# Kernel optimization log

Hardware: AMD Instinct MI355X
Metric: run time of the kernel (lower is better)

## Reference

```python
import jax, jax.numpy as jnp
import numpy as np

NUM_HEADS = 8
SCALE = 25.0
SIM_THRESH = 0.75


def setup_inputs() -> dict:
    key = jax.random.key(0)
    ks = jax.random.split(key, 6)
    B, N, C = 1, 2048, 1024
    x_cls = jax.random.normal(ks[0], (B, N, C), jnp.float32)
    x_reg = jax.random.normal(ks[1], (B, N, C), jnp.float32)
    cls_score = jax.random.uniform(ks[2], (N,), jnp.float32)
    fg_score = jax.random.uniform(ks[3], (N,), jnp.float32)
    W_qkv_cls = jax.random.normal(ks[4], (3 * C, C), jnp.float32) * 0.02
    W_qkv_reg = jax.random.normal(ks[5], (3 * C, C), jnp.float32) * 0.02
    return {"x_cls": x_cls, "x_reg": x_reg, "cls_score": cls_score,
            "fg_score": fg_score, "W_qkv_cls": W_qkv_cls, "W_qkv_reg": W_qkv_reg}


def _l2norm(t):
    return t / jnp.linalg.norm(t, axis=-1, keepdims=True)


def reference(x_cls, x_reg, cls_score, fg_score, W_qkv_cls, W_qkv_reg):
    B, N, C = x_cls.shape
    H = NUM_HEADS
    d = C // H

    def qkv(x, W):
        # (B,N,3C) -> (3,B,H,N,d)
        t = (x @ W.T).reshape(B, N, 3, H, d).transpose(2, 0, 3, 1, 4)
        return t[0], t[1], t[2]

    q_cls, k_cls, v_cls = qkv(x_cls, W_qkv_cls)
    q_reg, k_reg, _ = qkv(x_reg, W_qkv_reg)

    q_cls, k_cls = _l2norm(q_cls), _l2norm(k_cls)
    q_reg, k_reg = _l2norm(q_reg), _l2norm(k_reg)
    v_cls_normed = _l2norm(v_cls)

    # scores broadcast: s[..., i, j] = score[j]; transpose -> score[i]
    s_cls = cls_score.reshape(1, 1, 1, N)
    s_fg = fg_score.reshape(1, 1, 1, N)
    # use_mask=True branch
    m_cls = (s_cls > jnp.swapaxes(s_cls, -2, -1) - 0.1).astype(x_cls.dtype)
    m_fg = (s_fg > jnp.swapaxes(s_fg, -2, -1) - 0.1).astype(x_cls.dtype)

    attn_cls_raw = jnp.einsum('bhid,bhjd->bhij', v_cls_normed, v_cls_normed)

    attn_cls = jax.nn.softmax(
        jnp.einsum('bhid,bhjd->bhij', q_cls, k_cls) * SCALE * s_cls * m_cls, axis=-1)
    attn_reg = jax.nn.softmax(
        jnp.einsum('bhid,bhjd->bhij', q_reg, k_reg) * SCALE * s_fg * m_fg, axis=-1)
    attn = (attn_reg + attn_cls) * 0.5

    x = jnp.einsum('bhij,bhjd->bhid', attn, v_cls).transpose(0, 2, 1, 3).reshape(B, N, C)
    x_ori = v_cls.transpose(0, 2, 1, 3).reshape(B, N, C)
    x_out = jnp.concatenate([x, x_ori], axis=-1)  # (B, N, 2C)

    # ave=True branch (batch 0, head-mean)
    raw = attn_cls_raw.sum(axis=1)[0] / H  # (N, N)
    sim_mask = (raw > SIM_THRESH).astype(x_cls.dtype)
    sim_attn = attn.sum(axis=1)[0] / H
    sim_round2 = jax.nn.softmax(sim_attn, axis=-1)
    sim_round2 = sim_mask * sim_round2
    sim_round2 = sim_round2 / jnp.sum(sim_round2, axis=-1, keepdims=True)
    return x_out, sim_round2
```

## Files before the change

kernel.cpp:

```cpp
#include <hip/hip_runtime.h>


#define NTOK 2048
#define CDIM 1024
#define OD   5120

typedef __attribute__((ext_vector_type(8))) short bf16x8;
typedef __attribute__((ext_vector_type(4))) short s16x4;
typedef __attribute__((ext_vector_type(2))) short s16x2;
typedef __attribute__((ext_vector_type(4))) float f32x4;

#define MFMA16(a,b,c) __builtin_amdgcn_mfma_f32_16x16x32_bf16((a),(b),(c),0,0,0)

__device__ __forceinline__ short f2bf(float x){
  unsigned u = __float_as_uint(x);
  u += 0x7FFFu + ((u >> 16) & 1u);
  return (short)(u >> 16);
}

__device__ __forceinline__ void atomAddF(float* p, float v){
  unsafeAtomicAdd(p, v);
}

__device__ __forceinline__ void gld16(const short* g, short* l){
  __builtin_amdgcn_global_load_lds(
      (const __attribute__((address_space(1))) unsigned int*)g,
      (__attribute__((address_space(3))) unsigned int*)l, 16, 0, 0);
}

__global__ __launch_bounds__(256,2) void k_qkv(
    const float* __restrict__ xcls, const float* __restrict__ xreg,
    const float* __restrict__ Wcls, const float* __restrict__ Wreg,
    float* __restrict__ tmp)
{
  const int m0 = blockIdx.x * 64;
  const int o0 = blockIdx.y * 64;
  const float* X; const float* W; int wrow;
  if (o0 < 3072){ X = xcls; W = Wcls; wrow = o0; }
  else          { X = xreg; W = Wreg; wrow = o0 - 3072; }

  __shared__ short As[64][40];
  __shared__ short Bs[64][40];

  const int tid  = threadIdx.x;
  const int lane = tid & 63;
  const int wid  = tid >> 6;
  const int wm   = (wid >> 1) * 32;
  const int wo   = (wid & 1) * 32;
  const int fr   = lane & 15;
  const int fk   = (lane >> 4) * 8;

  f32x4 acc[2][2] = {};

  for (int k0 = 0; k0 < CDIM; k0 += 32){
    #pragma unroll
    for (int it = 0; it < 2; ++it){
      int idx = tid + it*256;
      int r = idx >> 3;
      int c = (idx & 7) << 2;
      float4 xv = *(const float4*)(X + (size_t)(m0+r)*CDIM + k0 + c);
      *(s16x4*)&As[r][c] = (s16x4){ f2bf(xv.x), f2bf(xv.y), f2bf(xv.z), f2bf(xv.w) };
      float4 wv = *(const float4*)(W + (size_t)(wrow+r)*CDIM + k0 + c);
      *(s16x4*)&Bs[r][c] = (s16x4){ f2bf(wv.x), f2bf(wv.y), f2bf(wv.z), f2bf(wv.w) };
    }
    __syncthreads();
    bf16x8 a0 = *(const bf16x8*)&As[wm      + fr][fk];
    bf16x8 a1 = *(const bf16x8*)&As[wm + 16 + fr][fk];
    bf16x8 b0 = *(const bf16x8*)&Bs[wo      + fr][fk];
    bf16x8 b1 = *(const bf16x8*)&Bs[wo + 16 + fr][fk];
    acc[0][0] = MFMA16(a0,b0,acc[0][0]);
    acc[0][1] = MFMA16(a0,b1,acc[0][1]);
    acc[1][0] = MFMA16(a1,b0,acc[1][0]);
    acc[1][1] = MFMA16(a1,b1,acc[1][1]);
    __syncthreads();
  }
  #pragma unroll
  for (int fi=0;fi<2;fi++)
    #pragma unroll
    for (int fj=0;fj<2;fj++)
      #pragma unroll
      for (int r=0;r<4;r++){
        int mm = m0 + wm + fi*16 + (lane>>4)*4 + r;
        int oo = o0 + wo + fj*16 + fr;
        tmp[(size_t)mm*OD + oo] = acc[fi][fj][r];
      }
}

__global__ __launch_bounds__(256,4) void k_norm(
    const float* __restrict__ tmp, float* __restrict__ out,
    short* __restrict__ qc, short* __restrict__ kc,
    short* __restrict__ qr, short* __restrict__ kr,
    short* __restrict__ vn, short* __restrict__ vb)
{
  int task = blockIdx.x*4 + (threadIdx.x>>6);
  int lane = threadIdx.x & 63;
  int n = task / 40;
  int rem = task - n*40;
  int chunk = rem >> 3;
  int h = rem & 7;
  const float* src = tmp + (size_t)n*OD + (chunk<<10) + h*128;
  float2 v = *(const float2*)(src + lane*2);
  float ss = v.x*v.x + v.y*v.y;
  #pragma unroll
  for (int m=1;m<64;m<<=1) ss += __shfl_xor(ss, m);
  float rn = 1.0f / sqrtf(ss);
  size_t base = ((size_t)h*NTOK + n)*128 + lane*2;
  s16x2 nv = { f2bf(v.x*rn), f2bf(v.y*rn) };
  switch(chunk){
    case 0: *(s16x2*)&qc[base] = nv; break;
    case 1: *(s16x2*)&kc[base] = nv; break;
    case 3: *(s16x2*)&qr[base] = nv; break;
    case 4: *(s16x2*)&kr[base] = nv; break;
    default: {
      *(s16x2*)&vn[base] = nv;
      *(s16x2*)&vb[base] = (s16x2){ f2bf(v.x), f2bf(v.y) };
      *(float2*)&out[(size_t)n*2048 + 1024 + h*128 + lane*2] = v;
      break;
    }
  }
}

__global__ __launch_bounds__(256,4) void k_vT(
    const short* __restrict__ vb, short* __restrict__ vT)
{
  int b = blockIdx.x;
  int h  = b >> 6;
  int nt = (b >> 1) & 31;
  int dt = b & 1;
  __shared__ short t[64][72];
  int tid = threadIdx.x;
  int r  = tid >> 2;
  int c0 = (tid & 3) << 4;
  #pragma unroll
  for (int u=0;u<2;u++){
    bf16x8 val = *(const bf16x8*)&vb[((size_t)h*NTOK + nt*64 + r)*128 + dt*64 + c0 + u*8];
    #pragma unroll
    for (int e=0;e<8;e++) t[r][c0+u*8+e] = val[e];
  }
  __syncthreads();
  #pragma unroll
  for (int u=0;u<2;u++){
    bf16x8 o;
    #pragma unroll
    for (int e=0;e<8;e++) o[e] = t[c0+u*8+e][r];
    *(bf16x8*)&vT[((size_t)h*128 + dt*64 + r)*NTOK + nt*64 + c0 + u*8] = o;
  }
}

#define JLEN 1024

__global__ __launch_bounds__(256,2) void k_attn(
    const short* __restrict__ qc, const short* __restrict__ kc,
    const short* __restrict__ qr, const short* __restrict__ kr,
    const short* __restrict__ vT,
    const float* __restrict__ csc, const float* __restrict__ fsc,
    float* __restrict__ s_cls, float* __restrict__ s_reg,
    float* __restrict__ Up)
{
  const int tid = threadIdx.x;
  const int l   = tid & 63;
  const int w   = tid >> 6;
  const int L    = blockIdx.x;
  const int xcd  = L & 7;
  const int slot = L >> 3;
  const int hs   = ((slot >> 5) << 3) | xcd;
  const int h    = hs >> 1;
  const int s    = hs & 1;
  const int rem  = slot & 31;
  const int js   = rem >> 4;
  const int ib   = rem & 15;

  const int iw  = ib * 128 + w * 32;
  const int fr  = l & 15;
  const int fk8 = (l >> 4) * 8;
  const size_t hN = (size_t)h * NTOK;
  const size_t hD = (size_t)h * 128;

  const short* Qp = s ? qr : qc;
  const short* Kp = s ? kr : kc;
  const float* sc = s ? fsc : csc;
  float* ssum     = s ? s_reg : s_cls;
  float* Ub       = Up + (size_t)(js*2 + s) * 2097152;

  __shared__ __align__(16) short Kbuf[2][4][4][64][8];
  __shared__ __align__(16) short Vbuf[2][8][2][64][8];
  __shared__ __align__(16) short Ebuf[4][2][2][64][8];

  const int t8 = w * 8;

#define STAGE(DB, JN) do {                                                   \
    _Pragma("unroll")                                                        \
    for (int q8=0; q8<8; ++q8){                                              \
      int t = t8 + q8;                                                       \
      if (t < 16){                                                           \
        int jf = t >> 2, kk = t & 3;                                         \
        gld16(Kp + (hN + (JN) + jf*16 + fr)*128 + kk*32 + fk8,               \
              &Kbuf[DB][jf][kk][0][0]);                                      \
      } else {                                                               \
        int u = t - 16, df = u >> 1, ks = u & 1;                             \
        gld16(vT + (hD + df*16 + fr)*2048 + (JN) + ks*32 + fk8,              \
              &Vbuf[DB][df][ks][0][0]);                                      \
      }                                                                      \
    }                                                                        \
  } while(0)

  bf16x8 aq[2][4];
  #pragma unroll
  for (int i2=0;i2<2;i2++)
    #pragma unroll
    for (int kk=0;kk<4;kk++)
      aq[i2][kk] = *(const bf16x8*)&Qp[(hN + iw + i2*16 + fr)*128 + kk*32 + fk8];

  float sci[2][4];
  #pragma unroll
  for (int i2=0;i2<2;i2++)
    #pragma unroll
    for (int r=0;r<4;r++)
      sci[i2][r] = sc[iw + i2*16 + (l>>4)*4 + r];

  f32x4 U[2][8] = {};
  float p[2][4] = {};

  const int ebyte = l & 7;
  const int ehi   = (l >> 3) & 1;
  const int jbase = js * JLEN;

  STAGE(0, jbase);
  __syncthreads();

  for (int jt = 0; jt < 16; ++jt){
    const int db = jt & 1;
    const int j0 = jbase + jt*64;
    if (jt < 15){ if (db) STAGE(0, j0 + 64); else STAGE(1, j0 + 64); }
    #pragma unroll
    for (int jf=0; jf<4; ++jf){
      f32x4 S0 = {}; f32x4 S1 = {};
      #pragma unroll
      for (int kk=0; kk<4; ++kk){
        bf16x8 b = *(const bf16x8*)&Kbuf[db][jf][kk][l][0];
        S0 = MFMA16(aq[0][kk], b, S0);
        S1 = MFMA16(aq[1][kk], b, S1);
      }
      float sj = sc[j0 + jf*16 + fr];
      float sj25 = 25.0f * sj;
      const int ks  = jf >> 1;
      const int sub = ((jf & 1) << 1) | ehi;
      #pragma unroll
      for (int r=0;r<4;r++){
        float e0 = (sj > sci[0][r]-0.1f) ? __expf(S0[r]*sj25) : 1.0f;
        float e1 = (sj > sci[1][r]-0.1f) ? __expf(S1[r]*sj25) : 1.0f;
        p[0][r] += e0; p[1][r] += e1;
        int lrow = (l>>4)*4 + r + (sub<<4);
        Ebuf[w][0][ks][lrow][ebyte] = f2bf(e0);
        Ebuf[w][1][ks][lrow][ebyte] = f2bf(e1);
      }
    }
    #pragma unroll
    for (int ks=0; ks<2; ++ks){
      bf16x8 ef0 = *(const bf16x8*)&Ebuf[w][0][ks][l][0];
      bf16x8 ef1 = *(const bf16x8*)&Ebuf[w][1][ks][l][0];
      #pragma unroll
      for (int df=0; df<8; ++df){
        bf16x8 bv = *(const bf16x8*)&Vbuf[db][df][ks][l][0];
        U[0][df] = MFMA16(ef0, bv, U[0][df]);
        U[1][df] = MFMA16(ef1, bv, U[1][df]);
      }
    }
    __syncthreads();
  }
#undef STAGE

  #pragma unroll
  for (int m=1;m<16;m<<=1)
    #pragma unroll
    for (int i2=0;i2<2;i2++)
      #pragma unroll
      for (int r=0;r<4;r++) p[i2][r] += __shfl_xor(p[i2][r], m);
  if (fr == 0){
    #pragma unroll
    for (int i2=0;i2<2;i2++)
      #pragma unroll
      for (int r=0;r<4;r++)
        atomAddF(&ssum[hN + iw + i2*16 + (l>>4)*4 + r], p[i2][r]);
  }
  #pragma unroll
  for (int i2=0;i2<2;i2++)
    #pragma unroll
    for (int df=0;df<8;df++)
      #pragma unroll
      for (int r=0;r<4;r++)
        Ub[(hN + iw + i2*16 + (l>>4)*4 + r)*128 + df*16 + fr] = U[i2][df][r];
}

__global__ __launch_bounds__(256,8) void k_attn_fin(
    const float* __restrict__ Up,
    const float* __restrict__ s_cls, const float* __restrict__ s_reg,
    float* __restrict__ out)
{
  int task = blockIdx.x*4 + (threadIdx.x>>6);
  int lane = threadIdx.x & 63;
  int h = task >> 11;
  int row = task & 2047;
  size_t b = (size_t)task*128 + lane*2;
  float2 c0 = *(const float2*)(Up + 0*2097152 + b);
  float2 r0 = *(const float2*)(Up + 1*2097152 + b);
  float2 c1 = *(const float2*)(Up + 2*2097152 + b);
  float2 r1 = *(const float2*)(Up + 3*2097152 + b);
  float isc = 0.5f/s_cls[task];
  float isr = 0.5f/s_reg[task];
  float2 o = { (c0.x+c1.x)*isc + (r0.x+r1.x)*isr,
               (c0.y+c1.y)*isc + (r0.y+r1.y)*isr };
  *(float2*)&out[(size_t)row*2048 + h*128 + lane*2] = o;
}

__global__ __launch_bounds__(256,2) void k_sim(
    const short* __restrict__ qc, const short* __restrict__ kc,
    const short* __restrict__ qr, const short* __restrict__ kr,
    const float* __restrict__ csc, const float* __restrict__ fsc,
    const float* __restrict__ s_cls, const float* __restrict__ s_reg,
    float* __restrict__ out)
{
  const int tid  = threadIdx.x;
  const int lane = tid & 63;
  const int w    = tid >> 6;
  const int i0w  = blockIdx.x * 128 + w * 32;
  const int j0   = blockIdx.y * 64;
  const int fr   = lane & 15;
  const int fk   = (lane >> 4) * 8;

  __shared__ __align__(16) short Bsh[2][16][64][8];

  float sjc[4], sjf[4];
  #pragma unroll
  for (int js=0;js<4;js++){ sjc[js]=csc[j0+js*16+fr]; sjf[js]=fsc[j0+js*16+fr]; }
  int rowb[2]; float sci[2][4], sfi[2][4];
  #pragma unroll
  for (int ri=0;ri<2;ri++){
    rowb[ri] = i0w + ri*16 + ((lane>>4)<<2);
    #pragma unroll
    for (int r=0;r<4;r++){ sci[ri][r]=csc[rowb[ri]+r]; sfi[ri][r]=fsc[rowb[ri]+r]; }
  }

  f32x4 sim[2][4] = {};

  for (int h=0; h<8; ++h){
    const size_t hb = (size_t)h * NTOK;
    bf16x8 aq[2][4], ar[2][4];
    #pragma unroll
    for (int ri=0;ri<2;ri++)
      #pragma unroll
      for (int kk=0;kk<4;kk++){
        aq[ri][kk] = *(const bf16x8*)&qc[(hb + i0w + ri*16 + fr)*128 + kk*32 + fk];
        ar[ri][kk] = *(const bf16x8*)&qr[(hb + i0w + ri*16 + fr)*128 + kk*32 + fk];
      }
    float iscl[2][4], isrl[2][4];
    #pragma unroll
    for (int ri=0;ri<2;ri++)
      #pragma unroll
      for (int r=0;r<4;r++){
        iscl[ri][r] = 1.0f/s_cls[hb + rowb[ri] + r];
        isrl[ri][r] = 1.0f/s_reg[hb + rowb[ri] + r];
      }
    __syncthreads();
    #pragma unroll
    for (int it=0; it<8; ++it){
      int slot = it*256 + tid;
      int str  = slot >> 10;
      int frag = (slot >> 6) & 15;
      int l    = slot & 63;
      int r    = (frag >> 2)*16 + (l & 15);
      int c    = (frag & 3)*32 + (l >> 4)*8;
      const short* gp = (str ? kr : kc) + (hb + j0 + r)*128 + c;
      *(bf16x8*)&Bsh[str][frag][l][0] = *(const bf16x8*)gp;
    }
    __syncthreads();
    #pragma unroll
    for (int js=0; js<4; ++js){
      bf16x8 bc[4], br[4];
      #pragma unroll
      for (int kk=0;kk<4;kk++){
        bc[kk] = *(const bf16x8*)&Bsh[0][js*4+kk][lane][0];
        br[kk] = *(const bf16x8*)&Bsh[1][js*4+kk][lane][0];
      }
      #pragma unroll
      for (int ri=0;ri<2;ri++){
        f32x4 Sc = {}; f32x4 Sr = {};
        #pragma unroll
        for (int kk=0;kk<4;kk++){
          Sc = MFMA16(aq[ri][kk], bc[kk], Sc);
          Sr = MFMA16(ar[ri][kk], br[kk], Sr);
        }
        #pragma unroll
        for (int r=0;r<4;r++){
          float ec = (sjc[js] > sci[ri][r]-0.1f) ? __expf(Sc[r]*(25.0f*sjc[js])) : 1.0f;
          float er = (sjf[js] > sfi[ri][r]-0.1f) ? __expf(Sr[r]*(25.0f*sjf[js])) : 1.0f;
          sim[ri][js][r] += ec*iscl[ri][r] + er*isrl[ri][r];
        }
      }
    }
  }
  #pragma unroll
  for (int ri=0;ri<2;ri++)
    #pragma unroll
    for (int js=0;js<4;js++)
      #pragma unroll
      for (int r=0;r<4;r++)
        out[4194304ull + (size_t)(rowb[ri]+r)*2048 + j0 + js*16 + fr]
            = sim[ri][js][r] * 0.0625f;
}

__global__ __launch_bounds__(256,4) void k_raw(
    const short* __restrict__ vn, unsigned char* __restrict__ mask)
{
  const int tid  = threadIdx.x;
  const int lane = tid & 63;
  const int w    = tid >> 6;
  const int i0w  = blockIdx.x * 128 + w * 32;
  const int j0   = blockIdx.y * 64;
  const int fr   = lane & 15;
  const int fk   = (lane >> 4) * 8;

  __shared__ __align__(16) short Bsh[16][64][8];

  f32x4 raw[2][4] = {};

  for (int cc=0; cc<8; ++cc){
    const size_t hb = (size_t)cc * NTOK;
    bf16x8 av[2][4];
    #pragma unroll
    for (int ri=0;ri<2;ri++)
      #pragma unroll
      for (int kk=0;kk<4;kk++)
        av[ri][kk] = *(const bf16x8*)&vn[(hb + i0w + ri*16 + fr)*128 + kk*32 + fk];
    __syncthreads();
    #pragma unroll
    for (int it=0; it<4; ++it){
      int slot = it*256 + tid;
      int frag = (slot >> 6) & 15;
      int l    = slot & 63;
      int r    = (frag >> 2)*16 + (l & 15);
      int c    = (frag & 3)*32 + (l >> 4)*8;
      *(bf16x8*)&Bsh[frag][l][0] = *(const bf16x8*)&vn[(hb + j0 + r)*128 + c];
    }
    __syncthreads();
    #pragma unroll
    for (int js=0; js<4; ++js){
      bf16x8 bv[4];
      #pragma unroll
      for (int kk=0;kk<4;kk++) bv[kk] = *(const bf16x8*)&Bsh[js*4+kk][lane][0];
      #pragma unroll
      for (int ri=0;ri<2;ri++)
        #pragma unroll
        for (int kk=0;kk<4;kk++)
          raw[ri][js] = MFMA16(av[ri][kk], bv[kk], raw[ri][js]);
    }
  }
  const int rb0 = i0w + ((lane>>4)<<2);
  #pragma unroll
  for (int ri=0;ri<2;ri++)
    #pragma unroll
    for (int js=0;js<4;js++)
      #pragma unroll
      for (int r=0;r<4;r++)
        mask[(size_t)(rb0 + ri*16 + r)*2048 + j0 + js*16 + fr]
            = raw[ri][js][r] > 6.0f ? 1 : 0;
}

__global__ __launch_bounds__(256,4) void k_final(
    float* __restrict__ out, const unsigned char* __restrict__ mask)
{
  int row  = blockIdx.x*4 + (threadIdx.x>>6);
  int lane = threadIdx.x & 63;
  float* sr = out + 4194304ull + (size_t)row*2048;
  const unsigned char* mr = mask + (size_t)row*2048;
  float v[32];
  float sum2 = 0.0f;
  #pragma unroll
  for (int c=0;c<32;c++){
    float e = __expf(sr[c*64 + lane]);
    v[c] = (mr[c*64 + lane] != 0) ? e : 0.0f;
    sum2 += v[c];
  }
  #pragma unroll
  for (int m=1;m<64;m<<=1) sum2 += __shfl_xor(sum2, m);
  float inv = 1.0f / sum2;
  #pragma unroll
  for (int c=0;c<32;c++) sr[c*64 + lane] = v[c]*inv;
}

extern "C" void kernel_launch(void* const* d_in, const int* in_sizes, int n_in,
                              void* d_out, int out_size, void* d_ws, size_t ws_size,
                              hipStream_t stream)
{
  const float* xcls = (const float*)d_in[0];
  const float* xreg = (const float*)d_in[1];
  const float* csc  = (const float*)d_in[2];
  const float* fsc  = (const float*)d_in[3];
  const float* Wc   = (const float*)d_in[4];
  const float* Wr   = (const float*)d_in[5];
  float* out = (float*)d_out;

  char* ws = (char*)d_ws;
  float* tmp          = (float*)ws;
  unsigned char* mask = (unsigned char*)ws;
  char* accbase       = ws + 4u*1024*1024;
  float* s_cls        = (float*)(accbase);
  float* s_reg        = (float*)(accbase + 65536);
  float* Up           = (float*)(accbase + 131072);
  short* qc = (short*)(ws + 41943040ull);
  short* kc = qc + 2097152;
  short* qr = kc + 2097152;
  short* kr = qr + 2097152;
  short* vn = kr + 2097152;
  short* vb = vn + 2097152;
  short* vT = vb + 2097152;

  k_qkv  <<<dim3(32,80), 256, 0, stream>>>(xcls, xreg, Wc, Wr, tmp);
  k_norm <<<20480,       256, 0, stream>>>(tmp, out, qc, kc, qr, kr, vn, vb);
  k_vT   <<<512,         256, 0, stream>>>(vb, vT);
  hipMemsetAsync(accbase, 0, 131072, stream);
  k_attn <<<512,         256, 0, stream>>>(qc, kc, qr, kr, vT, csc, fsc,
                                           s_cls, s_reg, Up);
  k_attn_fin <<<4096,    256, 0, stream>>>(Up, s_cls, s_reg, out);
  k_raw  <<<dim3(16,32), 256, 0, stream>>>(vn, mask);
  k_sim  <<<dim3(16,32), 256, 0, stream>>>(qc, kc, qr, kr, csc, fsc, s_cls, s_reg, out);
  k_final<<<512,         256, 0, stream>>>(out, mask);
}
```

Baseline: 295.3 us.

## Pre-convert QKV inputs to bf16 and use 128x128 double-buffered LDS-DMA GEMM

Adds a separate pass that converts the fp32 inputs and weights to bf16 once. The QKV projection GEMM is rewritten with 128x128 tiles, 4x4 MFMA fragments per wave, double-buffered global_load_lds staging and an XCD-aware block mapping. This is meant to remove the repeated fp32-to-bf16 conversion in every tile, raise arithmetic intensity and overlap loads with compute. In exchange it writes an extra bf16 copy of the inputs to workspace that aliases qc/kc (safe only because k_norm writes them later), and it uses more registers per thread.

After: 254.8 us. 13.7% less time.

```diff
diff --git a/kernel.cpp b/kernel.cpp
--- a/kernel.cpp
+++ b/kernel.cpp
@@ -28,62 +28,95 @@
       (__attribute__((address_space(3))) unsigned int*)l, 16, 0, 0);
 }
 
-__global__ __launch_bounds__(256,2) void k_qkv(
-    const float* __restrict__ xcls, const float* __restrict__ xreg,
-    const float* __restrict__ Wcls, const float* __restrict__ Wreg,
+__global__ __launch_bounds__(256,8) void k_cvt(
+    const float* __restrict__ xc, const float* __restrict__ xr,
+    const float* __restrict__ Wc, const float* __restrict__ Wr,
+    short* __restrict__ xbc, short* __restrict__ xbr,
+    short* __restrict__ wbc, short* __restrict__ wbr)
+{
+  int idx = blockIdx.x*256 + threadIdx.x;
+  const float* src; short* dst; int off;
+  if      (idx <  262144){ src = xc; dst = xbc; off = idx; }
+  else if (idx <  524288){ src = xr; dst = xbr; off = idx - 262144; }
+  else if (idx <  917504){ src = Wc; dst = wbc; off = idx - 524288; }
+  else                   { src = Wr; dst = wbr; off = idx - 917504; }
+  float4 a = *(const float4*)(src + (size_t)off*8);
+  float4 b = *(const float4*)(src + (size_t)off*8 + 4);
+  bf16x8 o = { f2bf(a.x), f2bf(a.y), f2bf(a.z), f2bf(a.w),
+               f2bf(b.x), f2bf(b.y), f2bf(b.z), f2bf(b.w) };
+  *(bf16x8*)(dst + (size_t)off*8) = o;
+}
+
+__global__ __launch_bounds__(256,3) void k_qkv(
+    const short* __restrict__ xbc, const short* __restrict__ xbr,
+    const short* __restrict__ wbc, const short* __restrict__ wbr,
     float* __restrict__ tmp)
 {
-  const int m0 = blockIdx.x * 64;
-  const int o0 = blockIdx.y * 64;
-  const float* X; const float* W; int wrow;
-  if (o0 < 3072){ X = xcls; W = Wcls; wrow = o0; }
-  else          { X = xreg; W = Wreg; wrow = o0 - 3072; }
-
-  __shared__ short As[64][40];
-  __shared__ short Bs[64][40];
-
-  const int tid  = threadIdx.x;
-  const int lane = tid & 63;
-  const int wid  = tid >> 6;
-  const int wm   = (wid >> 1) * 32;
-  const int wo   = (wid & 1) * 32;
-  const int fr   = lane & 15;
-  const int fk   = (lane >> 4) * 8;
-
-  f32x4 acc[2][2] = {};
-
-  for (int k0 = 0; k0 < CDIM; k0 += 32){
-    #pragma unroll
-    for (int it = 0; it < 2; ++it){
-      int idx = tid + it*256;
-      int r = idx >> 3;
-      int c = (idx & 7) << 2;
-      float4 xv = *(const float4*)(X + (size_t)(m0+r)*CDIM + k0 + c);
-      *(s16x4*)&As[r][c] = (s16x4){ f2bf(xv.x), f2bf(xv.y), f2bf(xv.z), f2bf(xv.w) };
-      float4 wv = *(const float4*)(W + (size_t)(wrow+r)*CDIM + k0 + c);
-      *(s16x4*)&Bs[r][c] = (s16x4){ f2bf(wv.x), f2bf(wv.y), f2bf(wv.z), f2bf(wv.w) };
-    }
+  const int tid = threadIdx.x;
+  const int l   = tid & 63;
+  const int w   = tid >> 6;
+  const int fr  = l & 15;
+  const int fk8 = (l >> 4) * 8;
+
+  const int L     = blockIdx.x;
+  const int xcd   = L & 7;
+  const int slot  = L >> 3;
+  const int panel = xcd*5 + (slot >> 4);
+  const int mb    = slot & 15;
+  const int m0    = mb * 128;
+  const int o0    = panel * 128;
+
+  const short* Xb; const short* Wb; int wrow;
+  if (o0 < 3072){ Xb = xbc; Wb = wbc; wrow = o0; }
+  else          { Xb = xbr; Wb = wbr; wrow = o0 - 3072; }
+
+  __shared__ __align__(16) short Ab[2][8][64][8];
+  __shared__ __align__(16) short Bb[2][8][64][8];
+
+  const int wr = w >> 1;
+  const int wc = w & 1;
+
+#define QSTAGE(DB, KN) do {                                                  \
+    _Pragma("unroll")                                                        \
+    for (int it=0; it<2; ++it){                                              \
+      int f = it*4 + w;                                                      \
+      gld16(Xb + (size_t)(m0  + f*16 + fr)*CDIM + (KN) + fk8,                \
+            &Ab[DB][f][0][0]);                                               \
+      gld16(Wb + (size_t)(wrow + f*16 + fr)*CDIM + (KN) + fk8,               \
+            &Bb[DB][f][0][0]);                                               \
+    }                                                                        \
+  } while(0)
+
+  f32x4 acc[4][4] = {};
+
+  QSTAGE(0, 0);
+  __syncthreads();
+
+  for (int kt = 0; kt < 32; ++kt){
+    const int db = kt & 1;
+    if (kt < 31){ if (db) QSTAGE(0, (kt+1)*32); else QSTAGE(1, (kt+1)*32); }
+    bf16x8 af[4], bfr[4];
+    #pragma unroll
+    for (int ai=0;ai<4;ai++) af[ai]  = *(const bf16x8*)&Ab[db][wr*4+ai][l][0];
+    #pragma unroll
+    for (int bj=0;bj<4;bj++) bfr[bj] = *(const bf16x8*)&Bb[db][wc*4+bj][l][0];
+    #pragma unroll
+    for (int ai=0;ai<4;ai++)
+      #pragma unroll
+      for (int bj=0;bj<4;bj++)
+        acc[ai][bj] = MFMA16(af[ai], bfr[bj], acc[ai][bj]);
     __syncthreads();
-    bf16x8 a0 = *(const bf16x8*)&As[wm      + fr][fk];
-    bf16x8 a1 = *(const bf16x8*)&As[wm + 16 + fr][fk];
-    bf16x8 b0 = *(const bf16x8*)&Bs[wo      + fr][fk];
-    bf16x8 b1 = *(const bf16x8*)&Bs[wo + 16 + fr][fk];
-    acc[0][0] = MFMA16(a0,b0,acc[0][0]);
-    acc[0][1] = MFMA16(a0,b1,acc[0][1]);
-    acc[1][0] = MFMA16(a1,b0,acc[1][0]);
-    acc[1][1] = MFMA16(a1,b1,acc[1][1]);
-    __syncthreads();
-  }
-  #pragma unroll
-  for (int fi=0;fi<2;fi++)
-    #pragma unroll
-    for (int fj=0;fj<2;fj++)
-      #pragma unroll
-      for (int r=0;r<4;r++){
-        int mm = m0 + wm + fi*16 + (lane>>4)*4 + r;
-        int oo = o0 + wo + fj*16 + fr;
-        tmp[(size_t)mm*OD + oo] = acc[fi][fj][r];
-      }
+  }
+#undef QSTAGE
+
+  #pragma unroll
+  for (int ai=0;ai<4;ai++)
+    #pragma unroll
+    for (int bj=0;bj<4;bj++)
+      #pragma unroll
+      for (int r=0;r<4;r++)
+        tmp[(size_t)(m0 + wr*64 + ai*16 + (l>>4)*4 + r)*OD
+            + o0 + wc*64 + bj*16 + fr] = acc[ai][bj][r];
 }
 
 __global__ __launch_bounds__(256,4) void k_norm(
@@ -514,8 +547,13 @@
   short* vn = kr + 2097152;
   short* vb = vn + 2097152;
   short* vT = vb + 2097152;
-
-  k_qkv  <<<dim3(32,80), 256, 0, stream>>>(xcls, xreg, Wc, Wr, tmp);
+  short* xbc = (short*)(ws + 41943040ull);
+  short* xbr = xbc + 2097152;
+  short* wbc = xbr + 2097152;
+  short* wbr = wbc + 3145728;
+
+  k_cvt  <<<4608,        256, 0, stream>>>(xcls, xreg, Wc, Wr, xbc, xbr, wbc, wbr);
+  k_qkv  <<<640,         256, 0, stream>>>(xbc, xbr, wbc, wbr, tmp);
   k_norm <<<20480,       256, 0, stream>>>(tmp, out, qc, kc, qr, kr, vn, vb);
   k_vT   <<<512,         256, 0, stream>>>(vb, vT);
   hipMemsetAsync(accbase, 0, 131072, stream);
```
